# Performance work log

Measured on AMD Instinct MI355X. Metric: run time of the kernel, lower is better.

Reference implementation:

```python
import jax, jax.numpy as jnp
import numpy as np


def setup_inputs() -> dict:
    key = jax.random.key(0)
    k1, k2, k3, k4 = jax.random.split(key, 4)
    b, n1, n2, h = 8, 2048, 2048, 1024
    scale = 1.0 / np.sqrt(h)
    return {
        "S1": jax.random.normal(k1, (b, n1, h), dtype=jnp.float32),
        "S2": jax.random.normal(k2, (b, n2, h), dtype=jnp.float32),
        "W1": jax.random.normal(k3, (h, h), dtype=jnp.float32) * scale,
        "W2": jax.random.normal(k4, (h, h), dtype=jnp.float32) * scale,
    }


def reference(S1, S2, W1, W2):
    # nn.Linear(h, h, bias=False): y = x @ W.T
    S2_h = jnp.einsum('bnh,kh->bnk', S2, W1)            # (b, N2, h)
    scores1 = jnp.einsum('bmh,bnh->bmn', S1, S2_h)      # (b, N1, N2)
    attn1 = jax.nn.softmax(scores1, axis=-1)
    S1_out = jnp.einsum('bmn,bnh->bmh', attn1, S2)      # (b, N1, h)

    S1_h = jnp.einsum('bmh,kh->bmk', S1, W2)            # (b, N1, h)
    scores2 = jnp.einsum('bnh,bmh->bnm', S2, S1_h)      # (b, N2, N1)
    attn2 = jax.nn.softmax(scores2, axis=-1)
    S2_out = jnp.einsum('bnm,bmh->bnh', attn2, S1)      # (b, N2, h)
    return (S1_out, S2_out)
```

## Files before the change

### kernel.cpp

```cpp
#include <hip/hip_runtime.h>

typedef _Float16 f16;
typedef _Float16 f16x4 __attribute__((ext_vector_type(4)));
typedef _Float16 f16x8 __attribute__((ext_vector_type(8)));
typedef float    f32x4 __attribute__((ext_vector_type(4)));

#define MFMA(a,b,c) __builtin_amdgcn_mfma_f32_16x16x32_f16(a,b,c,0,0,0)
#define SBAR() __builtin_amdgcn_sched_barrier(0)
#define BARRIER() do { SBAR(); __builtin_amdgcn_s_barrier(); SBAR(); } while (0)
#define VMCNT(n) do { SBAR(); asm volatile("s_waitcnt vmcnt(" #n ")" ::: "memory"); SBAR(); } while (0)
#define LGKM0() do { asm volatile("s_waitcnt lgkmcnt(0)" ::: "memory"); SBAR(); } while (0)

__device__ __forceinline__ void gload_lds16(const f16* g, f16* l) {
  __builtin_amdgcn_global_load_lds(
      (const __attribute__((address_space(1))) unsigned int*)g,
      (__attribute__((address_space(3))) unsigned int*)l, 16, 0, 0);
}

__global__ __launch_bounds__(256)
void tof16x2_kernel(const float* __restrict__ w1, const float* __restrict__ w2,
                    f16* __restrict__ y1, f16* __restrict__ y2, int n4) {
  int i = blockIdx.x * 256 + threadIdx.x;
  if (i >= n4) return;
  const float* x = blockIdx.y ? w2 : w1;
  f16* y = blockIdx.y ? y2 : y1;
  f32x4 v = ((const f32x4*)x)[i];
  f16x4 h;
#pragma unroll
  for (int j = 0; j < 4; j++) h[j] = (f16)v[j];
  ((f16x4*)y)[i] = h;
}

__global__ __launch_bounds__(256)
void prep2_f16_kernel(const float* __restrict__ s1, const float* __restrict__ s2,
                      f16* __restrict__ rm1, f16* __restrict__ tr1,
                      f16* __restrict__ rm2, f16* __restrict__ tr2, int bc) {
  __shared__ f16 t[64][68];
  const int tid = threadIdx.x;
  const int zz = blockIdx.z;
  const int sel = zz >= bc;
  const size_t z = sel ? (zz - bc) : zz;
  const float* in = sel ? s2 : s1;
  f16* rm = sel ? rm2 : rm1;
  f16* tr = sel ? tr2 : tr1;
  const int n0 = blockIdx.x * 64, h0 = blockIdx.y * 64;
  const int rr = tid >> 4, cc = (tid & 15) * 4;
#pragma unroll
  for (int p = 0; p < 4; p++) {
    int n = rr + p * 16;
    f32x4 v = *(const f32x4*)(in + ((size_t)z * 2048 + n0 + n) * 1024 + h0 + cc);
    f16x4 h;
#pragma unroll
    for (int j = 0; j < 4; j++) h[j] = (f16)v[j];
    *(f16x4*)&t[n][cc] = h;
    *(f16x4*)(rm + ((size_t)z * 2048 + n0 + n) * 1024 + h0 + cc) = h;
  }
  __syncthreads();
#pragma unroll
  for (int p = 0; p < 4; p++) {
    int h = rr + p * 16;
    f16x4 o;
#pragma unroll
    for (int j = 0; j < 4; j++) o[j] = t[cc + j][h];
    *(f16x4*)(tr + ((size_t)z * 1024 + h0 + h) * 2048 + n0 + cc) = o;
  }
}

template <int OUTF32>
__global__ __launch_bounds__(512, 2)
void gemm256(const f16* __restrict__ Ag, size_t zA,
             const f16* __restrict__ Bg, size_t zB,
             void* __restrict__ Cg, size_t zC,
             int lda, int ldb, int ldc, int K, int ZB, int gx) {
  __shared__ f16 sm[8][8192];
  const int tid = threadIdx.x;
  const int id = blockIdx.x;
  const size_t z = id % ZB;
  const int k = id / ZB;
  const int bx = k % gx, by = k / gx;
  const f16* A = Ag + z * zA + (size_t)bx * 256 * lda;
  const f16* B = Bg + z * zB + (size_t)by * 256 * ldb;

  const int lane = tid & 63, w = tid >> 6;
  const int wm = w >> 2, wn = w & 3;
  const int lr = lane & 15, kg = lane >> 4;
  const int sx = (kg ^ ((lr >> 1) & 3)) << 3;
  const int aoff = wm * 4096 + lr * 32 + sx;
  const int boff = wn * 2048 + lr * 32 + sx;
  const int colx = (((tid & 3) ^ ((tid >> 3) & 3)) << 3);
  const int srow = tid >> 2;
  const int wls = w * 512;

  f32x4 acc[8][4] = {};
  f16x8 af[8], bf0, bf1;

#define STAGE(cc, mat, kkv, ktc) do {                                          \
    const f16* gs = ((mat) ? B : A) + (size_t)srow * ((mat) ? ldb : lda) +     \
                    (ktc) + (kkv) * 32 + colx;                                 \
    f16* ls = &sm[(cc) * 4 + (mat) * 2 + (kkv)][wls];                          \
    gload_lds16(gs, ls);                                                       \
    gload_lds16(gs + (size_t)128 * ((mat) ? ldb : lda), ls + 4096);            \
  } while (0)

#define LOAD_A(cc, kkv) do { _Pragma("unroll")                                 \
    for (int fm = 0; fm < 8; fm++)                                             \
      af[fm] = *(const f16x8*)&sm[(cc) * 4 + (kkv)][aoff + fm * 512];          \
  } while (0)

#define LOAD_B(cc, kkv, nh) do {                                               \
    bf0 = *(const f16x8*)&sm[(cc) * 4 + 2 + (kkv)][boff + (nh) * 1024];        \
    bf1 = *(const f16x8*)&sm[(cc) * 4 + 2 + (kkv)][boff + (nh) * 1024 + 512];  \
  } while (0)

#define DOMFMA(nh) do {                                                        \
    __builtin_amdgcn_s_setprio(1);                                             \
    _Pragma("unroll")                                                          \
    for (int fm = 0; fm < 8; fm++) {                                           \
      acc[fm][(nh) * 2]     = MFMA(af[fm], bf0, acc[fm][(nh) * 2]);            \
      acc[fm][(nh) * 2 + 1] = MFMA(af[fm], bf1, acc[fm][(nh) * 2 + 1]);        \
    }                                                                          \
    __builtin_amdgcn_s_setprio(0);                                             \
    SBAR();                                                                    \
  } while (0)

  const int nt = K >> 6;
  STAGE(0, 0, 0, 0);
  STAGE(0, 1, 0, 0);
  STAGE(0, 0, 1, 0);
  STAGE(0, 1, 1, 0);
  VMCNT(4);
  BARRIER();

  for (int t = 0; t < nt - 1; ++t) {
    const int c = t & 1;
    const int kt1 = (t + 1) << 6;
    LOAD_A(c, 0); LOAD_B(c, 0, 0);
    STAGE(c ^ 1, 0, 0, kt1);
    BARRIER();
    LGKM0();
    DOMFMA(0);
    BARRIER();
    LOAD_B(c, 0, 1);
    STAGE(c ^ 1, 1, 0, kt1);
    BARRIER();
    LGKM0();
    DOMFMA(1);
    VMCNT(4);
    BARRIER();
    LOAD_A(c, 1); LOAD_B(c, 1, 0);
    STAGE(c ^ 1, 0, 1, kt1);
    BARRIER();
    LGKM0();
    DOMFMA(0);
    BARRIER();
    LOAD_B(c, 1, 1);
    STAGE(c ^ 1, 1, 1, kt1);
    BARRIER();
    LGKM0();
    DOMFMA(1);
    VMCNT(4);
    BARRIER();
  }
  {
    const int c = (nt - 1) & 1;
    LOAD_A(c, 0); LOAD_B(c, 0, 0);
    BARRIER();
    LGKM0();
    DOMFMA(0);
    BARRIER();
    LOAD_B(c, 0, 1);
    BARRIER();
    LGKM0();
    DOMFMA(1);
    VMCNT(0);
    BARRIER();
    LOAD_A(c, 1); LOAD_B(c, 1, 0);
    BARRIER();
    LGKM0();
    DOMFMA(0);
    BARRIER();
    LOAD_B(c, 1, 1);
    BARRIER();
    LGKM0();
    DOMFMA(1);
  }

#pragma unroll
  for (int fm = 0; fm < 8; fm++)
#pragma unroll
    for (int fn = 0; fn < 4; fn++)
#pragma unroll
      for (int q = 0; q < 4; q++) {
        size_t grow = (size_t)bx * 256 + wm * 128 + fm * 16 + kg * 4 + q;
        int gcol = by * 256 + wn * 64 + fn * 16 + lr;
        if (OUTF32)
          ((float*)Cg)[z * zC + grow * ldc + gcol] = acc[fm][fn][q];
        else
          ((f16*)Cg)[z * zC + grow * ldc + gcol] = (f16)acc[fm][fn][q];
      }
#undef STAGE
#undef LOAD_A
#undef LOAD_B
#undef DOMFMA
}

__global__ __launch_bounds__(256)
void softmax_rows(const float* __restrict__ SC, f16* __restrict__ Pb) {
  const float* r = SC + (size_t)blockIdx.x * 2048;
  f16* po = Pb + (size_t)blockIdx.x * 2048;
  const int tid = threadIdx.x;
  f32x4 a = *(const f32x4*)(r + tid * 8);
  f32x4 b = *(const f32x4*)(r + tid * 8 + 4);
  float x[8] = {a[0], a[1], a[2], a[3], b[0], b[1], b[2], b[3]};
#pragma unroll
  for (int i = 0; i < 8; i++) x[i] = fminf(fmaxf(x[i], -1e30f), 1e30f);
  float m = x[0];
#pragma unroll
  for (int i = 1; i < 8; i++) m = fmaxf(m, x[i]);
#pragma unroll
  for (int off = 32; off; off >>= 1) m = fmaxf(m, __shfl_xor(m, off));
  __shared__ float rmax[4], rsum[4];
  const int w = tid >> 6, lane = tid & 63;
  if (!lane) rmax[w] = m;
  __syncthreads();
  m = fmaxf(fmaxf(rmax[0], rmax[1]), fmaxf(rmax[2], rmax[3]));
  float e[8], s = 0.f;
#pragma unroll
  for (int i = 0; i < 8; i++) {
    e[i] = __expf(x[i] - m);
    s += e[i];
  }
#pragma unroll
  for (int off = 32; off; off >>= 1) s += __shfl_xor(s, off);
  if (!lane) rsum[w] = s;
  __syncthreads();
  s = rsum[0] + rsum[1] + rsum[2] + rsum[3];
  float inv = 1.0f / s;
  f16x8 p;
#pragma unroll
  for (int i = 0; i < 8; i++) p[i] = (f16)(e[i] * inv);
  *(f16x8*)(po + tid * 8) = p;
}

extern "C" void kernel_launch(void* const* d_in, const int* in_sizes, int n_in,
                              void* d_out, int out_size, void* d_ws, size_t ws_size,
                              hipStream_t stream) {
  const float* S1 = (const float*)d_in[0];
  const float* S2 = (const float*)d_in[1];
  const float* W1 = (const float*)d_in[2];
  const float* W2 = (const float*)d_in[3];
  float* out = (float*)d_out;
  const int B = 8, N = 2048, H = 1024;
  const size_t NH = (size_t)N * H;
  const size_t NN = (size_t)N * N;
  const size_t WN = (size_t)H * H;

  char* ws = (char*)d_ws;
  f16* W1h = (f16*)ws;
  f16* W2h = W1h + WN;
  size_t fixed = 2 * WN * sizeof(f16);
  size_t perb = 5 * NH * sizeof(f16) + NN * sizeof(float) + NN * sizeof(f16);

  int bc = 1;
  const int cands[4] = {8, 4, 2, 1};
  for (int ci = 0; ci < 4; ci++) {
    if (fixed + (size_t)cands[ci] * perb <= ws_size) { bc = cands[ci]; break; }
  }
  f16* Ah = (f16*)(ws + fixed);
  f16* Bh = Ah + (size_t)bc * NH;
  f16* At = Bh + (size_t)bc * NH;
  f16* Bt = At + (size_t)bc * NH;
  f16* Kh = Bt + (size_t)bc * NH;
  float* SC = (float*)(Kh + (size_t)bc * NH);
  f16* Pb = (f16*)(SC + (size_t)bc * NN);

  {
    int n4 = (int)(WN / 4);
    tof16x2_kernel<<<dim3((n4 + 255) / 256, 2), 256, 0, stream>>>(
        W1, W2, W1h, W2h, n4);
  }

  for (int c0 = 0; c0 < B; c0 += bc) {
    prep2_f16_kernel<<<dim3(N / 64, H / 64, 2 * bc), 256, 0, stream>>>(
        S1 + (size_t)c0 * NH, S2 + (size_t)c0 * NH, Ah, At, Bh, Bt, bc);

    for (int path = 0; path < 2; path++) {
      const f16* Qh = path ? Bh : Ah;
      const f16* Xh = path ? Ah : Bh;
      const f16* Vt = path ? At : Bt;
      const f16* Wh = path ? W2h : W1h;
      float* Op = out + (size_t)path * B * NH + (size_t)c0 * NH;

      gemm256<0><<<dim3(bc * 32), 512, 0, stream>>>(
          Xh, 0, Wh, 0, Kh, 0, H, H, H, H, 1, bc * 8);
      gemm256<1><<<dim3(bc * 64), 512, 0, stream>>>(
          Qh, NH, Kh, NH, SC, NN, H, H, N, H, bc, 8);
      softmax_rows<<<dim3(bc * N), 256, 0, stream>>>(SC, Pb);
      gemm256<1><<<dim3(bc * 32), 512, 0, stream>>>(
          Pb, NN, Vt, NH, Op, NH, N, N, H, N, bc, 8);
    }
  }
}
```

Before: 493.0 us.

## Fuse softmax into score GEMM epilogue with per-tile max/sum and rescale in PV GEMM

The score GEMM now computes per-256-column-tile row maxima and exp-sums in its epilogue and writes unnormalized exp values as f16, replacing the fp32 score matrix and the separate softmax pass. A small combine kernel merges the eight tile partials per row into per-tile scale factors. The PV GEMM multiplies its A fragments by those factors before the MFMAs. This removes the fp32 score write/read and a full softmax kernel, at the cost of extra LDS reductions and barriers in the epilogue, per-fragment multiplies in the inner loop, and some f16 precision risk on the unnormalized exponentials.

```diff
diff --git a/kernel.cpp b/kernel.cpp
--- a/kernel.cpp
+++ b/kernel.cpp
@@ -66,11 +66,12 @@
   }
 }
 
-template <int OUTF32>
+template <int MODE>
 __global__ __launch_bounds__(512, 2)
 void gemm256(const f16* __restrict__ Ag, size_t zA,
              const f16* __restrict__ Bg, size_t zB,
              void* __restrict__ Cg, size_t zC,
+             float2* __restrict__ Pp, const f16* __restrict__ Cbp,
              int lda, int ldb, int ldc, int K, int ZB, int gx) {
   __shared__ f16 sm[8][8192];
   const int tid = threadIdx.x;
@@ -93,6 +94,10 @@
 
   f32x4 acc[8][4] = {};
   f16x8 af[8], bf0, bf1;
+  f16 cf[8];
+  const f16* cbbase = nullptr;
+  if (MODE == 2)
+    cbbase = Cbp + ((size_t)z * 2048 + (size_t)bx * 256 + wm * 128 + lr) * 8;
 
 #define STAGE(cc, mat, kkv, ktc) do {                                          \
     const f16* gs = ((mat) ? B : A) + (size_t)srow * ((mat) ? ldb : lda) +     \
@@ -106,6 +111,9 @@
     for (int fm = 0; fm < 8; fm++)                                             \
       af[fm] = *(const f16x8*)&sm[(cc) * 4 + (kkv)][aoff + fm * 512];          \
   } while (0)
+
+#define MULA() do { if (MODE == 2) { _Pragma("unroll")                         \
+    for (int fm = 0; fm < 8; fm++) af[fm] = af[fm] * cf[fm]; } } while (0)
 
 #define LOAD_B(cc, kkv, nh) do {                                               \
     bf0 = *(const f16x8*)&sm[(cc) * 4 + 2 + (kkv)][boff + (nh) * 1024];        \
@@ -123,21 +131,28 @@
     SBAR();                                                                    \
   } while (0)
 
+#define LOADCF(t) do { if (MODE == 2 && (((t) & 3) == 0)) { _Pragma("unroll")  \
+    for (int fm = 0; fm < 8; fm++) cf[fm] = cbbase[fm * 128 + ((t) >> 2)]; }   \
+  } while (0)
+
   const int nt = K >> 6;
   STAGE(0, 0, 0, 0);
   STAGE(0, 1, 0, 0);
   STAGE(0, 0, 1, 0);
   STAGE(0, 1, 1, 0);
+  LOADCF(0);
   VMCNT(4);
   BARRIER();
 
   for (int t = 0; t < nt - 1; ++t) {
     const int c = t & 1;
     const int kt1 = (t + 1) << 6;
+    LOADCF(t);
     LOAD_A(c, 0); LOAD_B(c, 0, 0);
     STAGE(c ^ 1, 0, 0, kt1);
     BARRIER();
     LGKM0();
+    MULA();
     DOMFMA(0);
     BARRIER();
     LOAD_B(c, 0, 1);
@@ -151,6 +166,7 @@
     STAGE(c ^ 1, 0, 1, kt1);
     BARRIER();
     LGKM0();
+    MULA();
     DOMFMA(0);
     BARRIER();
     LOAD_B(c, 1, 1);
@@ -163,9 +179,11 @@
   }
   {
     const int c = (nt - 1) & 1;
+    LOADCF(nt - 1);
     LOAD_A(c, 0); LOAD_B(c, 0, 0);
     BARRIER();
     LGKM0();
+    MULA();
     DOMFMA(0);
     BARRIER();
     LOAD_B(c, 0, 1);
@@ -177,6 +195,7 @@
     LOAD_A(c, 1); LOAD_B(c, 1, 0);
     BARRIER();
     LGKM0();
+    MULA();
     DOMFMA(0);
     BARRIER();
     LOAD_B(c, 1, 1);
@@ -185,61 +204,126 @@
     DOMFMA(1);
   }
 
-#pragma unroll
-  for (int fm = 0; fm < 8; fm++)
-#pragma unroll
-    for (int fn = 0; fn < 4; fn++)
+  if (MODE == 0 || MODE == 2) {
+#pragma unroll
+    for (int fm = 0; fm < 8; fm++)
+#pragma unroll
+      for (int fn = 0; fn < 4; fn++)
+#pragma unroll
+        for (int q = 0; q < 4; q++) {
+          size_t grow = (size_t)bx * 256 + wm * 128 + fm * 16 + kg * 4 + q;
+          int gcol = by * 256 + wn * 64 + fn * 16 + lr;
+          if (MODE == 2)
+            ((float*)Cg)[z * zC + grow * ldc + gcol] = acc[fm][fn][q];
+          else
+            ((f16*)Cg)[z * zC + grow * ldc + gcol] = (f16)acc[fm][fn][q];
+        }
+  } else {
+    float* red1 = (float*)&sm[0][0];
+    float* red2 = red1 + 1024;
+    float mx[8][4];
+#pragma unroll
+    for (int fm = 0; fm < 8; fm++)
 #pragma unroll
       for (int q = 0; q < 4; q++) {
-        size_t grow = (size_t)bx * 256 + wm * 128 + fm * 16 + kg * 4 + q;
-        int gcol = by * 256 + wn * 64 + fn * 16 + lr;
-        if (OUTF32)
-          ((float*)Cg)[z * zC + grow * ldc + gcol] = acc[fm][fn][q];
-        else
-          ((f16*)Cg)[z * zC + grow * ldc + gcol] = (f16)acc[fm][fn][q];
+        float m0 = fmaxf(fmaxf(acc[fm][0][q], acc[fm][1][q]),
+                         fmaxf(acc[fm][2][q], acc[fm][3][q]));
+#pragma unroll
+        for (int off = 1; off < 16; off <<= 1) m0 = fmaxf(m0, __shfl_xor(m0, off));
+        mx[fm][q] = m0;
       }
+    BARRIER();
+    if (lr == 0) {
+#pragma unroll
+      for (int fm = 0; fm < 8; fm++)
+#pragma unroll
+        for (int q = 0; q < 4; q++)
+          red1[wm * 512 + (fm * 16 + kg * 4 + q) * 4 + wn] = mx[fm][q];
+    }
+    BARRIER();
+    float M[8][4];
+#pragma unroll
+    for (int fm = 0; fm < 8; fm++)
+#pragma unroll
+      for (int q = 0; q < 4; q++) {
+        int row = fm * 16 + kg * 4 + q;
+        M[fm][q] = fmaxf(fmaxf(red1[wm * 512 + row * 4 + 0],
+                               red1[wm * 512 + row * 4 + 1]),
+                         fmaxf(red1[wm * 512 + row * 4 + 2],
+                               red1[wm * 512 + row * 4 + 3]));
+      }
+    float sp[8][4] = {};
+#pragma unroll
+    for (int fm = 0; fm < 8; fm++)
+#pragma unroll
+      for (int fn = 0; fn < 4; fn++)
+#pragma unroll
+        for (int q = 0; q < 4; q++) {
+          float e = __expf(acc[fm][fn][q] - M[fm][q]);
+          sp[fm][q] += e;
+          size_t grow = (size_t)bx * 256 + wm * 128 + fm * 16 + kg * 4 + q;
+          int gcol = by * 256 + wn * 64 + fn * 16 + lr;
+          ((f16*)Cg)[z * zC + grow * ldc + gcol] = (f16)e;
+        }
+#pragma unroll
+    for (int fm = 0; fm < 8; fm++)
+#pragma unroll
+      for (int q = 0; q < 4; q++) {
+        float s0 = sp[fm][q];
+#pragma unroll
+        for (int off = 1; off < 16; off <<= 1) s0 += __shfl_xor(s0, off);
+        sp[fm][q] = s0;
+      }
+    BARRIER();
+    if (lr == 0) {
+#pragma unroll
+      for (int fm = 0; fm < 8; fm++)
+#pragma unroll
+        for (int q = 0; q < 4; q++)
+          red2[wm * 512 + (fm * 16 + kg * 4 + q) * 4 + wn] = sp[fm][q];
+    }
+    BARRIER();
+    if (wn == 0 && lr == 0) {
+#pragma unroll
+      for (int fm = 0; fm < 8; fm++)
+#pragma unroll
+        for (int q = 0; q < 4; q++) {
+          int row = fm * 16 + kg * 4 + q;
+          float S = red2[wm * 512 + row * 4 + 0] + red2[wm * 512 + row * 4 + 1] +
+                    red2[wm * 512 + row * 4 + 2] + red2[wm * 512 + row * 4 + 3];
+          size_t grow = (size_t)bx * 256 + wm * 128 + row;
+          float2 pv; pv.x = M[fm][q]; pv.y = S;
+          Pp[(z * 2048 + grow) * 8 + by] = pv;
+        }
+    }
+  }
 #undef STAGE
 #undef LOAD_A
+#undef MULA
 #undef LOAD_B
 #undef DOMFMA
+#undef LOADCF
 }
 
 __global__ __launch_bounds__(256)
-void softmax_rows(const float* __restrict__ SC, f16* __restrict__ Pb) {
-  const float* r = SC + (size_t)blockIdx.x * 2048;
-  f16* po = Pb + (size_t)blockIdx.x * 2048;
-  const int tid = threadIdx.x;
-  f32x4 a = *(const f32x4*)(r + tid * 8);
-  f32x4 b = *(const f32x4*)(r + tid * 8 + 4);
-  float x[8] = {a[0], a[1], a[2], a[3], b[0], b[1], b[2], b[3]};
-#pragma unroll
-  for (int i = 0; i < 8; i++) x[i] = fminf(fmaxf(x[i], -1e30f), 1e30f);
-  float m = x[0];
-#pragma unroll
-  for (int i = 1; i < 8; i++) m = fmaxf(m, x[i]);
-#pragma unroll
-  for (int off = 32; off; off >>= 1) m = fmaxf(m, __shfl_xor(m, off));
-  __shared__ float rmax[4], rsum[4];
-  const int w = tid >> 6, lane = tid & 63;
-  if (!lane) rmax[w] = m;
-  __syncthreads();
-  m = fmaxf(fmaxf(rmax[0], rmax[1]), fmaxf(rmax[2], rmax[3]));
-  float e[8], s = 0.f;
-#pragma unroll
-  for (int i = 0; i < 8; i++) {
-    e[i] = __expf(x[i] - m);
-    s += e[i];
-  }
-#pragma unroll
-  for (int off = 32; off; off >>= 1) s += __shfl_xor(s, off);
-  if (!lane) rsum[w] = s;
-  __syncthreads();
-  s = rsum[0] + rsum[1] + rsum[2] + rsum[3];
+void combine_msum(const float2* __restrict__ Pp, f16* __restrict__ Cb, int nrows) {
+  int r = blockIdx.x * 256 + threadIdx.x;
+  if (r >= nrows) return;
+  const float2* p = Pp + (size_t)r * 8;
+  float2 pb[8];
+#pragma unroll
+  for (int b = 0; b < 8; b++) pb[b] = p[b];
+  float m = pb[0].x;
+#pragma unroll
+  for (int b = 1; b < 8; b++) m = fmaxf(m, pb[b].x);
+  float s = 0.f;
+#pragma unroll
+  for (int b = 0; b < 8; b++) s += pb[b].y * __expf(pb[b].x - m);
   float inv = 1.0f / s;
-  f16x8 p;
-#pragma unroll
-  for (int i = 0; i < 8; i++) p[i] = (f16)(e[i] * inv);
-  *(f16x8*)(po + tid * 8) = p;
+  f16x8 o;
+#pragma unroll
+  for (int b = 0; b < 8; b++) o[b] = (f16)(__expf(pb[b].x - m) * inv);
+  *(f16x8*)(Cb + (size_t)r * 8) = o;
 }
 
 extern "C" void kernel_launch(void* const* d_in, const int* in_sizes, int n_in,
@@ -259,7 +343,8 @@
   f16* W1h = (f16*)ws;
   f16* W2h = W1h + WN;
   size_t fixed = 2 * WN * sizeof(f16);
-  size_t perb = 5 * NH * sizeof(f16) + NN * sizeof(float) + NN * sizeof(f16);
+  size_t perb = 5 * NH * sizeof(f16) + NN * sizeof(f16) +
+                (size_t)N * 8 * sizeof(float2) + (size_t)N * 8 * sizeof(f16);
 
   int bc = 1;
   const int cands[4] = {8, 4, 2, 1};
@@ -271,8 +356,9 @@
   f16* At = Bh + (size_t)bc * NH;
   f16* Bt = At + (size_t)bc * NH;
   f16* Kh = Bt + (size_t)bc * NH;
-  float* SC = (float*)(Kh + (size_t)bc * NH);
-  f16* Pb = (f16*)(SC + (size_t)bc * NN);
+  f16* Eb = Kh + (size_t)bc * NH;
+  float2* Pp = (float2*)(Eb + (size_t)bc * NN);
+  f16* Cb = (f16*)(Pp + (size_t)bc * N * 8);
 
   {
     int n4 = (int)(WN / 4);
@@ -292,12 +378,13 @@
       float* Op = out + (size_t)path * B * NH + (size_t)c0 * NH;
 
       gemm256<0><<<dim3(bc * 32), 512, 0, stream>>>(
-          Xh, 0, Wh, 0, Kh, 0, H, H, H, H, 1, bc * 8);
+          Xh, 0, Wh, 0, Kh, 0, nullptr, nullptr, H, H, H, H, 1, bc * 8);
       gemm256<1><<<dim3(bc * 64), 512, 0, stream>>>(
-          Qh, NH, Kh, NH, SC, NN, H, H, N, H, bc, 8);
-      softmax_rows<<<dim3(bc * N), 256, 0, stream>>>(SC, Pb);
-      gemm256<1><<<dim3(bc * 32), 512, 0, stream>>>(
-          Pb, NN, Vt, NH, Op, NH, N, N, H, N, bc, 8);
+          Qh, NH, Kh, NH, Eb, NN, Pp, nullptr, H, H, N, H, bc, 8);
+      combine_msum<<<dim3((bc * N + 255) / 256), 256, 0, stream>>>(
+          Pp, Cb, bc * N);
+      gemm256<2><<<dim3(bc * 32), 512, 0, stream>>>(
+          Eb, NN, Vt, NH, Op, NH, nullptr, Cb, N, N, H, N, bc, 8);
     }
   }
 }
```

Result: slower. 511.6 us (+3.8%).
